# Kernel tuning notes

Hardware: AMD Instinct MI355X
Metric: run time of the kernel (lower is better)

## Reference

```python
import jax, jax.numpy as jnp
import numpy as np


def setup_inputs() -> dict:
    key = jax.random.key(0)
    ks = jax.random.split(key, 7)
    B, C, H, W = 8, 256, 64, 64
    C8 = C // 8
    s = 0.05
    return {
        "x": jax.random.normal(ks[0], (B, C, H, W), dtype=jnp.float32),
        "wq": jax.random.normal(ks[1], (C8, C), dtype=jnp.float32) * s,
        "bq": jax.random.normal(ks[2], (C8,), dtype=jnp.float32) * s,
        "wk": jax.random.normal(ks[3], (C8, C), dtype=jnp.float32) * s,
        "bk": jax.random.normal(ks[4], (C8,), dtype=jnp.float32) * s,
        "wv": jax.random.normal(ks[5], (C, C), dtype=jnp.float32) * s,
        "bv": jax.random.normal(ks[6], (C,), dtype=jnp.float32) * s,
    }


def reference(x, wq, bq, wk, bk, wv, bv):
    B, C, H, W = x.shape
    xf = x.reshape(B, C, H * W)                      # [B, C, N]
    # conv1x1 projections (per-position linear over channels)
    f = jnp.einsum('oc,bcn->bon', wq, xf) + bq[None, :, None]   # [B, C/8, N]
    g = jnp.einsum('oc,bcn->bon', wk, xf) + bk[None, :, None]   # [B, C/8, N]
    h = jnp.einsum('oc,bcn->bon', wv, xf) + bv[None, :, None]   # [B, C,   N]
    # scores[b, n, m] = sum_c f[b,c,n] * g[b,c,m]  == bmm(f^T, g)
    scores = jnp.einsum('bcn,bcm->bnm', f, g)        # [B, N, N]
    # NOTE: original uses softmax over dim=1 (the f/query-position axis)
    beta = jax.nn.softmax(scores, axis=1)            # [B, N, N]
    # o[b, c, m] = sum_n h[b,c,n] * beta[b,n,m]  == bmm(h, beta)
    o = jnp.einsum('bcn,bnm->bcm', h, beta)          # [B, C, N]
    return o.reshape(B, C, H, W)
```

## Files before the change

### kernel.cpp

```cpp
#include <hip/hip_runtime.h>
#include <hip/hip_bf16.h>

typedef __bf16 bf16_t;
typedef __bf16 bf16x8 __attribute__((ext_vector_type(8)));
typedef __bf16 bf16x4 __attribute__((ext_vector_type(4)));
typedef float  f32x4  __attribute__((ext_vector_type(4)));

#define NB  8
#define NC  256
#define NC8 32
#define NN  4096
#define XS  264

#define MFMA16(a, b, c) __builtin_amdgcn_mfma_f32_16x16x32_bf16((a), (b), (c), 0, 0, 0)

__global__ __launch_bounds__(256) void cvt_all(const float* __restrict__ wq,
                                               const float* __restrict__ wk,
                                               const float* __restrict__ wv,
                                               bf16_t* __restrict__ wqb,
                                               bf16_t* __restrict__ wkb,
                                               bf16_t* __restrict__ wvb) {
    int i = blockIdx.x * 256 + threadIdx.x;
    const float* src; bf16_t* dst; int off;
    if (i < 2048)      { src = wq; dst = wqb; off = i; }
    else if (i < 4096) { src = wk; dst = wkb; off = i - 2048; }
    else               { src = wv; dst = wvb; off = i - 4096; }
    float4 v = reinterpret_cast<const float4*>(src)[off];
    bf16x4 o;
    o[0] = (bf16_t)v.x; o[1] = (bf16_t)v.y; o[2] = (bf16_t)v.z; o[3] = (bf16_t)v.w;
    reinterpret_cast<bf16x4*>(dst)[off] = o;
}

__global__ __launch_bounds__(256) void proj_fused(const float* __restrict__ x,
                                                  const bf16_t* __restrict__ wq,
                                                  const float* __restrict__ bq,
                                                  const bf16_t* __restrict__ wk,
                                                  const float* __restrict__ bk,
                                                  const bf16_t* __restrict__ wv,
                                                  const float* __restrict__ bv,
                                                  bf16_t* __restrict__ ft,
                                                  bf16_t* __restrict__ gt,
                                                  bf16_t* __restrict__ h) {
    __shared__ bf16_t tile[64][72];
    __shared__ bf16_t xs[64 * XS];

    const int bx = blockIdx.x;
    const int b  = bx >> 6;
    const int n0 = (bx & 63) * 64;
    const int t  = threadIdx.x;
    const int w    = t >> 6;
    const int lane = t & 63;
    const int q    = lane >> 4;
    const int r    = lane & 15;

    const int cl  = t >> 4;
    const int nl  = (t & 15) * 4;
    const int nb_ = t >> 3;
    const int cl2 = (t & 7) * 8;

    float4 xv[16];
#pragma unroll
    for (int cp = 0; cp < 4; ++cp)
#pragma unroll
        for (int p = 0; p < 4; ++p)
            xv[4 * cp + p] = *reinterpret_cast<const float4*>(
                x + ((size_t)b * NC + 64 * cp + cl + 16 * p) * NN + n0 + nl);

    for (int cp = 0; cp < 4; ++cp) {
#pragma unroll
        for (int p = 0; p < 4; ++p) {
            const int cc = cl + 16 * p;
            float4 v = xv[4 * cp + p];
            bf16x4 bv4;
            bv4[0] = (bf16_t)v.x; bv4[1] = (bf16_t)v.y; bv4[2] = (bf16_t)v.z; bv4[3] = (bf16_t)v.w;
            *reinterpret_cast<bf16x4*>(&tile[cc][nl]) = bv4;
        }
        __syncthreads();
#pragma unroll
        for (int p = 0; p < 2; ++p) {
            const int nn = nb_ + 32 * p;
            bf16x8 v;
            for (int i = 0; i < 8; ++i) v[i] = tile[cl2 + i][nn];
            *reinterpret_cast<bf16x8*>(&xs[nn * XS + 64 * cp + cl2]) = v;
        }
        __syncthreads();
    }

    {
        const bf16_t* xrow = &xs[(16 * w + r) * XS];
        f32x4 accq[2], acck[2];
        for (int ot = 0; ot < 2; ++ot) {
            accq[ot] = (f32x4){0.f, 0.f, 0.f, 0.f};
            acck[ot] = (f32x4){0.f, 0.f, 0.f, 0.f};
        }
        bf16x8 a_c  = *reinterpret_cast<const bf16x8*>(xrow + 8 * q);
        bf16x8 fq_c[2], fk_c[2];
#pragma unroll
        for (int ot = 0; ot < 2; ++ot) {
            fq_c[ot] = *reinterpret_cast<const bf16x8*>(wq + (size_t)(16 * ot + r) * NC + 8 * q);
            fk_c[ot] = *reinterpret_cast<const bf16x8*>(wk + (size_t)(16 * ot + r) * NC + 8 * q);
        }
        for (int k0 = 0; k0 < NC; k0 += 32) {
            const int kn = (k0 + 32 < NC) ? k0 + 32 : 0;
            bf16x8 a_n = *reinterpret_cast<const bf16x8*>(xrow + kn + 8 * q);
            bf16x8 fq_n[2], fk_n[2];
#pragma unroll
            for (int ot = 0; ot < 2; ++ot) {
                fq_n[ot] = *reinterpret_cast<const bf16x8*>(wq + (size_t)(16 * ot + r) * NC + kn + 8 * q);
                fk_n[ot] = *reinterpret_cast<const bf16x8*>(wk + (size_t)(16 * ot + r) * NC + kn + 8 * q);
            }
#pragma unroll
            for (int ot = 0; ot < 2; ++ot) {
                accq[ot] = MFMA16(a_c, fq_c[ot], accq[ot]);
                acck[ot] = MFMA16(a_c, fk_c[ot], acck[ot]);
            }
            a_c = a_n;
#pragma unroll
            for (int ot = 0; ot < 2; ++ot) { fq_c[ot] = fq_n[ot]; fk_c[ot] = fk_n[ot]; }
        }
        for (int ot = 0; ot < 2; ++ot) {
            const int o = 16 * ot + r;
            const float biq = bq[o];
            const float bik = bk[o];
            for (int i = 0; i < 4; ++i) {
                const int n = n0 + 16 * w + 4 * q + i;
                ft[((size_t)b * NN + n) * NC8 + o] = (bf16_t)(accq[ot][i] + biq);
                gt[((size_t)b * NN + n) * NC8 + o] = (bf16_t)(acck[ot][i] + bik);
            }
        }
    }

    f32x4 vacc[4][4];
    for (int ct = 0; ct < 4; ++ct)
        for (int nt = 0; nt < 4; ++nt) vacc[ct][nt] = (f32x4){0.f, 0.f, 0.f, 0.f};

    bf16x8 wv_c[4];
#pragma unroll
    for (int ct = 0; ct < 4; ++ct)
        wv_c[ct] = *reinterpret_cast<const bf16x8*>(
            wv + (size_t)(64 * ct + 16 * w + r) * NC + 8 * q);

    for (int k0 = 0; k0 < NC; k0 += 32) {
        const int kn = (k0 + 32 < NC) ? k0 + 32 : 0;
        bf16x8 wv_n[4];
#pragma unroll
        for (int ct = 0; ct < 4; ++ct)
            wv_n[ct] = *reinterpret_cast<const bf16x8*>(
                wv + (size_t)(64 * ct + 16 * w + r) * NC + kn + 8 * q);
        bf16x8 bfr[4];
#pragma unroll
        for (int nt = 0; nt < 4; ++nt)
            bfr[nt] = *reinterpret_cast<const bf16x8*>(&xs[(16 * nt + r) * XS + k0 + 8 * q]);
#pragma unroll
        for (int ct = 0; ct < 4; ++ct)
#pragma unroll
            for (int nt = 0; nt < 4; ++nt)
                vacc[ct][nt] = MFMA16(wv_c[ct], bfr[nt], vacc[ct][nt]);
#pragma unroll
        for (int ct = 0; ct < 4; ++ct) wv_c[ct] = wv_n[ct];
    }
    for (int ct = 0; ct < 4; ++ct) {
        for (int nt = 0; nt < 4; ++nt) {
            const int n32 = (n0 >> 5) + (nt >> 1);
            const int dn  = 16 * (nt & 1) + r;
            for (int i = 0; i < 4; ++i) {
                const int c = 64 * ct + 16 * w + 4 * q + i;
                h[(((size_t)b * 128 + n32) * NC + c) * 32 + dn] = (bf16_t)(vacc[ct][nt][i] + bv[c]);
            }
        }
    }
}

#define O_STEP(HU, HL, KC, LOFF)                                               \
    {                                                                          \
        _Pragma("unroll")                                                      \
        for (int ct = 0; ct < 2; ++ct)                                         \
            HL[ct] = *reinterpret_cast<const bf16x8*>(                         \
                hrow[ct] + (size_t)(LOFF) * 256);                              \
        bf16x8 pf[4];                                                          \
        _Pragma("unroll")                                                      \
        for (int mt = 0; mt < 4; ++mt) {                                       \
            const int row = 16 * mt + r;                                       \
            pf[mt] = *reinterpret_cast<const bf16x8*>(                         \
                &Pb[(row << 7) + (((4 * (KC) + q) ^ rq) << 3)]);               \
        }                                                                      \
        _Pragma("unroll")                                                      \
        for (int ct = 0; ct < 2; ++ct)                                         \
            _Pragma("unroll")                                                  \
            for (int mt = 0; mt < 4; ++mt)                                     \
                acc[ct][mt] = MFMA16(HU[ct], pf[mt], acc[ct][mt]);             \
    }

__global__ __launch_bounds__(512, 4) void attn(const bf16_t* __restrict__ ft,
                                               const bf16_t* __restrict__ gt,
                                               const bf16_t* __restrict__ h,
                                               float* __restrict__ out) {
    __shared__ bf16_t P[2 * 64 * 128];
    __shared__ float  l_lds[64];

    const int bx = blockIdx.x;
    const int b  = bx & 7;
    const int m0 = (bx >> 3) * 64;
    const int tid  = threadIdx.x;
    const int w    = tid >> 6;
    const int lane = tid & 63;
    const int q    = lane >> 4;
    const int r    = lane & 15;
    const int rq   = r & 7;

    if (tid < 64) l_lds[tid] = 0.f;

    bf16x8 qf[4];
#pragma unroll
    for (int mt = 0; mt < 4; ++mt)
        qf[mt] = *reinterpret_cast<const bf16x8*>(
            gt + ((size_t)b * NN + m0 + 16 * mt + r) * NC8 + 8 * q);

    f32x4 acc[2][4];
#pragma unroll
    for (int ct = 0; ct < 2; ++ct)
#pragma unroll
        for (int mt = 0; mt < 4; ++mt) acc[ct][mt] = (f32x4){0.f, 0.f, 0.f, 0.f};
    float lp[4] = {0.f, 0.f, 0.f, 0.f};

    const bf16_t* fb = ft + (size_t)b * NN * NC8;
    const bf16_t* hb = h + (size_t)b * 128 * NC * 32;
    const f32x4 zero = (f32x4){0.f, 0.f, 0.f, 0.f};

    const bf16_t* hrow[2];
#pragma unroll
    for (int ct = 0; ct < 2; ++ct)
        hrow[ct] = hb + (size_t)(32 * w + 16 * ct + r) * 32 + 8 * q;
    const bf16_t* fptr = fb + (size_t)(16 * w + r) * NC8 + 8 * q;

    f32x4 s[4];
    {
        bf16x8 a0 = *reinterpret_cast<const bf16x8*>(fptr);
#pragma unroll
        for (int mt = 0; mt < 4; ++mt) s[mt] = MFMA16(a0, qf[mt], zero);
    }
    bf16x8 h0[2], h1[2];
#pragma unroll
    for (int ct = 0; ct < 2; ++ct)
        h0[ct] = *reinterpret_cast<const bf16x8*>(hrow[ct]);

    for (int ii = 0; ii < 32; ++ii) {
        bf16_t* Pb = &P[(ii & 1) << 13];
        const int nb = ii * 128;
        const int nld = (ii + 1 < 32 ? ii + 1 : 31) * 128;

        bf16x8 af0 = *reinterpret_cast<const bf16x8*>(fptr + (size_t)nld * NC8);

#pragma unroll
        for (int mt = 0; mt < 4; ++mt) {
            float e0 = __expf(s[mt][0]);
            float e1 = __expf(s[mt][1]);
            float e2 = __expf(s[mt][2]);
            float e3 = __expf(s[mt][3]);
            lp[mt] += (e0 + e1) + (e2 + e3);
            bf16x4 pv;
            pv[0] = (bf16_t)e0; pv[1] = (bf16_t)e1; pv[2] = (bf16_t)e2; pv[3] = (bf16_t)e3;
            const int row  = 16 * mt + r;
            const int nblk = 2 * w + (q >> 1);
            *reinterpret_cast<bf16x4*>(
                &Pb[(row << 7) + ((nblk ^ rq) << 3) + 4 * (q & 1)]) = pv;
        }

        asm volatile("s_waitcnt lgkmcnt(0)" ::: "memory");
        __builtin_amdgcn_sched_barrier(0);
        __builtin_amdgcn_s_barrier();
        __builtin_amdgcn_sched_barrier(0);

        const int nbn = (ii + 1 < 32 ? nb + 128 : nb);
        __builtin_amdgcn_s_setprio(1);
        O_STEP(h0, h1, 0, nb + 32);
        O_STEP(h1, h0, 1, nb + 64);
        O_STEP(h0, h1, 2, nb + 96);
        O_STEP(h1, h0, 3, nbn);

#pragma unroll
        for (int mt = 0; mt < 4; ++mt) s[mt] = MFMA16(af0, qf[mt], zero);
        __builtin_amdgcn_s_setprio(0);
    }

    __syncthreads();
#pragma unroll
    for (int mt = 0; mt < 4; ++mt) {
        float v = lp[mt];
        v += __shfl_xor(v, 16);
        v += __shfl_xor(v, 32);
        if (q == 0) atomicAdd(&l_lds[16 * mt + r], v);
    }
    __syncthreads();

#pragma unroll
    for (int ct = 0; ct < 2; ++ct) {
#pragma unroll
        for (int mt = 0; mt < 4; ++mt) {
            const int m = m0 + 16 * mt + r;
            const float linv = 1.0f / l_lds[16 * mt + r];
#pragma unroll
            for (int i = 0; i < 4; ++i) {
                const int c = 32 * w + 16 * ct + 4 * q + i;
                out[((size_t)b * NC + c) * NN + m] = acc[ct][mt][i] * linv;
            }
        }
    }
}

extern "C" void kernel_launch(void* const* d_in, const int* in_sizes, int n_in,
                              void* d_out, int out_size, void* d_ws, size_t ws_size,
                              hipStream_t stream) {
    const float* x  = (const float*)d_in[0];
    const float* wq = (const float*)d_in[1];
    const float* bq = (const float*)d_in[2];
    const float* wk = (const float*)d_in[3];
    const float* bk = (const float*)d_in[4];
    const float* wv = (const float*)d_in[5];
    const float* bv = (const float*)d_in[6];
    float* out = (float*)d_out;

    bf16_t* ft  = (bf16_t*)d_ws;
    bf16_t* gt  = ft + (size_t)NB * NN * NC8;
    bf16_t* hb  = gt + (size_t)NB * NN * NC8;
    bf16_t* wqb = hb + (size_t)NB * NC * NN;
    bf16_t* wkb = wqb + (size_t)NC8 * NC;
    bf16_t* wvb = wkb + (size_t)NC8 * NC;

    cvt_all<<<80, 256, 0, stream>>>(wq, wk, wv, wqb, wkb, wvb);
    proj_fused<<<NB * (NN / 64), 256, 0, stream>>>(x, wqb, bq, wkb, bk, wvb, bv, ft, gt, hb);
    attn<<<NB * (NN / 64), 512, 0, stream>>>(ft, gt, hb, out);
}
```

Baseline: 191.8 us.

## Split projection into separate transpose kernel and global-memory projection matmul

Moves the x transpose and bf16 conversion out of the fused projection kernel into a dedicated kernel that writes a transposed bf16 copy of x into the output buffer as scratch. The projection kernel then reads its MFMA operands directly from global memory instead of LDS, with register double-buffering of the x fragments. The aim is to cut LDS usage and barrier stalls in the projection kernel so more blocks fit per CU. The cost is an extra kernel launch and a full write and re-read of the transposed x through global memory.

```diff
diff --git a/kernel.cpp b/kernel.cpp
--- a/kernel.cpp
+++ b/kernel.cpp
@@ -31,19 +31,69 @@
     reinterpret_cast<bf16x4*>(dst)[off] = o;
 }
 
-__global__ __launch_bounds__(256) void proj_fused(const float* __restrict__ x,
-                                                  const bf16_t* __restrict__ wq,
-                                                  const float* __restrict__ bq,
-                                                  const bf16_t* __restrict__ wk,
-                                                  const float* __restrict__ bk,
-                                                  const bf16_t* __restrict__ wv,
-                                                  const float* __restrict__ bv,
-                                                  bf16_t* __restrict__ ft,
-                                                  bf16_t* __restrict__ gt,
-                                                  bf16_t* __restrict__ h) {
+__global__ __launch_bounds__(256) void xpose(const float* __restrict__ x,
+                                             bf16_t* __restrict__ xt) {
     __shared__ bf16_t tile[64][72];
     __shared__ bf16_t xs[64 * XS];
 
+    const int bx = blockIdx.x;
+    const int b  = bx >> 6;
+    const int n0 = (bx & 63) * 64;
+    const int t  = threadIdx.x;
+
+    const int cl  = t >> 4;
+    const int nl  = (t & 15) * 4;
+    const int nb_ = t >> 3;
+    const int cl2 = (t & 7) * 8;
+
+    float4 xv[16];
+#pragma unroll
+    for (int cp = 0; cp < 4; ++cp)
+#pragma unroll
+        for (int p = 0; p < 4; ++p)
+            xv[4 * cp + p] = *reinterpret_cast<const float4*>(
+                x + ((size_t)b * NC + 64 * cp + cl + 16 * p) * NN + n0 + nl);
+
+    for (int cp = 0; cp < 4; ++cp) {
+#pragma unroll
+        for (int p = 0; p < 4; ++p) {
+            const int cc = cl + 16 * p;
+            float4 v = xv[4 * cp + p];
+            bf16x4 bv4;
+            bv4[0] = (bf16_t)v.x; bv4[1] = (bf16_t)v.y; bv4[2] = (bf16_t)v.z; bv4[3] = (bf16_t)v.w;
+            *reinterpret_cast<bf16x4*>(&tile[cc][nl]) = bv4;
+        }
+        __syncthreads();
+#pragma unroll
+        for (int p = 0; p < 2; ++p) {
+            const int nn = nb_ + 32 * p;
+            bf16x8 v;
+            for (int i = 0; i < 8; ++i) v[i] = tile[cl2 + i][nn];
+            *reinterpret_cast<bf16x8*>(&xs[nn * XS + 64 * cp + cl2]) = v;
+        }
+        __syncthreads();
+    }
+
+    const int row = t >> 5;
+    const int ch  = t & 31;
+#pragma unroll
+    for (int p = 0; p < 8; ++p) {
+        const int rr = row + 8 * p;
+        bf16x8 v = *reinterpret_cast<const bf16x8*>(&xs[rr * XS + ch * 8]);
+        *reinterpret_cast<bf16x8*>(xt + ((size_t)b * NN + n0 + rr) * NC + ch * 8) = v;
+    }
+}
+
+__global__ __launch_bounds__(256) void projmm(const bf16_t* __restrict__ xt,
+                                              const bf16_t* __restrict__ wq,
+                                              const float* __restrict__ bq,
+                                              const bf16_t* __restrict__ wk,
+                                              const float* __restrict__ bk,
+                                              const bf16_t* __restrict__ wv,
+                                              const float* __restrict__ bv,
+                                              bf16_t* __restrict__ ft,
+                                              bf16_t* __restrict__ gt,
+                                              bf16_t* __restrict__ h) {
     const int bx = blockIdx.x;
     const int b  = bx >> 6;
     const int n0 = (bx & 63) * 64;
@@ -53,41 +103,10 @@
     const int q    = lane >> 4;
     const int r    = lane & 15;
 
-    const int cl  = t >> 4;
-    const int nl  = (t & 15) * 4;
-    const int nb_ = t >> 3;
-    const int cl2 = (t & 7) * 8;
-
-    float4 xv[16];
-#pragma unroll
-    for (int cp = 0; cp < 4; ++cp)
-#pragma unroll
-        for (int p = 0; p < 4; ++p)
-            xv[4 * cp + p] = *reinterpret_cast<const float4*>(
-                x + ((size_t)b * NC + 64 * cp + cl + 16 * p) * NN + n0 + nl);
-
-    for (int cp = 0; cp < 4; ++cp) {
-#pragma unroll
-        for (int p = 0; p < 4; ++p) {
-            const int cc = cl + 16 * p;
-            float4 v = xv[4 * cp + p];
-            bf16x4 bv4;
-            bv4[0] = (bf16_t)v.x; bv4[1] = (bf16_t)v.y; bv4[2] = (bf16_t)v.z; bv4[3] = (bf16_t)v.w;
-            *reinterpret_cast<bf16x4*>(&tile[cc][nl]) = bv4;
-        }
-        __syncthreads();
-#pragma unroll
-        for (int p = 0; p < 2; ++p) {
-            const int nn = nb_ + 32 * p;
-            bf16x8 v;
-            for (int i = 0; i < 8; ++i) v[i] = tile[cl2 + i][nn];
-            *reinterpret_cast<bf16x8*>(&xs[nn * XS + 64 * cp + cl2]) = v;
-        }
-        __syncthreads();
-    }
+    const bf16_t* xb = xt + ((size_t)b * NN + n0) * NC;
 
     {
-        const bf16_t* xrow = &xs[(16 * w + r) * XS];
+        const bf16_t* xrow = xb + (size_t)(16 * w + r) * NC;
         f32x4 accq[2], acck[2];
         for (int ot = 0; ot < 2; ++ot) {
             accq[ot] = (f32x4){0.f, 0.f, 0.f, 0.f};
@@ -134,30 +153,34 @@
     for (int ct = 0; ct < 4; ++ct)
         for (int nt = 0; nt < 4; ++nt) vacc[ct][nt] = (f32x4){0.f, 0.f, 0.f, 0.f};
 
-    bf16x8 wv_c[4];
+    bf16x8 wv_c[4], bfr_c[4];
 #pragma unroll
     for (int ct = 0; ct < 4; ++ct)
         wv_c[ct] = *reinterpret_cast<const bf16x8*>(
             wv + (size_t)(64 * ct + 16 * w + r) * NC + 8 * q);
+#pragma unroll
+    for (int nt = 0; nt < 4; ++nt)
+        bfr_c[nt] = *reinterpret_cast<const bf16x8*>(xb + (size_t)(16 * nt + r) * NC + 8 * q);
 
     for (int k0 = 0; k0 < NC; k0 += 32) {
         const int kn = (k0 + 32 < NC) ? k0 + 32 : 0;
-        bf16x8 wv_n[4];
+        bf16x8 wv_n[4], bfr_n[4];
 #pragma unroll
         for (int ct = 0; ct < 4; ++ct)
             wv_n[ct] = *reinterpret_cast<const bf16x8*>(
                 wv + (size_t)(64 * ct + 16 * w + r) * NC + kn + 8 * q);
-        bf16x8 bfr[4];
 #pragma unroll
         for (int nt = 0; nt < 4; ++nt)
-            bfr[nt] = *reinterpret_cast<const bf16x8*>(&xs[(16 * nt + r) * XS + k0 + 8 * q]);
+            bfr_n[nt] = *reinterpret_cast<const bf16x8*>(xb + (size_t)(16 * nt + r) * NC + kn + 8 * q);
 #pragma unroll
         for (int ct = 0; ct < 4; ++ct)
 #pragma unroll
             for (int nt = 0; nt < 4; ++nt)
-                vacc[ct][nt] = MFMA16(wv_c[ct], bfr[nt], vacc[ct][nt]);
+                vacc[ct][nt] = MFMA16(wv_c[ct], bfr_c[nt], vacc[ct][nt]);
 #pragma unroll
         for (int ct = 0; ct < 4; ++ct) wv_c[ct] = wv_n[ct];
+#pragma unroll
+        for (int nt = 0; nt < 4; ++nt) bfr_c[nt] = bfr_n[nt];
     }
     for (int ct = 0; ct < 4; ++ct) {
         for (int nt = 0; nt < 4; ++nt) {
@@ -327,7 +350,10 @@
     bf16_t* wkb = wqb + (size_t)NC8 * NC;
     bf16_t* wvb = wkb + (size_t)NC8 * NC;
 
+    bf16_t* xT = (bf16_t*)out;
+
     cvt_all<<<80, 256, 0, stream>>>(wq, wk, wv, wqb, wkb, wvb);
-    proj_fused<<<NB * (NN / 64), 256, 0, stream>>>(x, wqb, bq, wkb, bk, wvb, bv, ft, gt, hb);
+    xpose<<<NB * (NN / 64), 256, 0, stream>>>(x, xT);
+    projmm<<<NB * (NN / 64), 256, 0, stream>>>(xT, wqb, bq, wkb, bk, wvb, bv, ft, gt, hb);
     attn<<<NB * (NN / 64), 512, 0, stream>>>(ft, gt, hb, out);
 }
```

Measured after the change: 203.1 us. 5.9% more time.

## Pre-tile bf16 weights and swap MFMA operands for vectorized projection stores

Applied to the files above, without the earlier changes.

The weight conversion kernel now writes bf16 weights in a 16x32 tiled layout, so each lane's 8-element fragment load is contiguous within a tile. The projection kernel swaps the MFMA A/B operands so every lane's accumulators hold four consecutive output channels (q/k) or positions (v), which allows bf16x4 vector stores instead of scalar ones. Weight fragments are prefetched before the x transpose, and the xs LDS fragments are double-buffered. This targets scattered global stores and weight-load latency in the projection stage only, leaving the attention kernel, which is likely the dominant cost, unchanged.

```diff
diff --git a/kernel.cpp b/kernel.cpp
--- a/kernel.cpp
+++ b/kernel.cpp
@@ -13,6 +13,7 @@
 #define XS  264
 
 #define MFMA16(a, b, c) __builtin_amdgcn_mfma_f32_16x16x32_bf16((a), (b), (c), 0, 0, 0)
+
 
 __global__ __launch_bounds__(256) void cvt_all(const float* __restrict__ wq,
                                                const float* __restrict__ wk,
@@ -26,21 +27,25 @@
     else if (i < 4096) { src = wk; dst = wkb; off = i - 2048; }
     else               { src = wv; dst = wvb; off = i - 4096; }
     float4 v = reinterpret_cast<const float4*>(src)[off];
-    bf16x4 o;
-    o[0] = (bf16_t)v.x; o[1] = (bf16_t)v.y; o[2] = (bf16_t)v.z; o[3] = (bf16_t)v.w;
-    reinterpret_cast<bf16x4*>(dst)[off] = o;
+    const int e = off * 4;
+    const int o = e >> 8;
+    const int k = e & 255;
+    const size_t d = (size_t)((o >> 4) * 8 + (k >> 5)) * 512 + (o & 15) * 32 + (k & 31);
+    bf16x4 ov;
+    ov[0] = (bf16_t)v.x; ov[1] = (bf16_t)v.y; ov[2] = (bf16_t)v.z; ov[3] = (bf16_t)v.w;
+    *reinterpret_cast<bf16x4*>(dst + d) = ov;
 }
 
-__global__ __launch_bounds__(256) void proj_fused(const float* __restrict__ x,
-                                                  const bf16_t* __restrict__ wq,
-                                                  const float* __restrict__ bq,
-                                                  const bf16_t* __restrict__ wk,
-                                                  const float* __restrict__ bk,
-                                                  const bf16_t* __restrict__ wv,
-                                                  const float* __restrict__ bv,
-                                                  bf16_t* __restrict__ ft,
-                                                  bf16_t* __restrict__ gt,
-                                                  bf16_t* __restrict__ h) {
+__global__ __launch_bounds__(256) void proj2(const float* __restrict__ x,
+                                             const bf16_t* __restrict__ wq,
+                                             const float* __restrict__ bq,
+                                             const bf16_t* __restrict__ wk,
+                                             const float* __restrict__ bk,
+                                             const bf16_t* __restrict__ wv,
+                                             const float* __restrict__ bv,
+                                             bf16_t* __restrict__ ft,
+                                             bf16_t* __restrict__ gt,
+                                             bf16_t* __restrict__ h) {
     __shared__ bf16_t tile[64][72];
     __shared__ bf16_t xs[64 * XS];
 
@@ -66,6 +71,18 @@
             xv[4 * cp + p] = *reinterpret_cast<const float4*>(
                 x + ((size_t)b * NC + 64 * cp + cl + 16 * p) * NN + n0 + nl);
 
+    const int fo = r * 32 + 8 * q;
+    bf16x8 fq_c[2], fk_c[2], wv_c[4];
+#pragma unroll
+    for (int ot = 0; ot < 2; ++ot) {
+        fq_c[ot] = *reinterpret_cast<const bf16x8*>(wq + ot * 4096 + fo);
+        fk_c[ot] = *reinterpret_cast<const bf16x8*>(wk + ot * 4096 + fo);
+    }
+#pragma unroll
+    for (int ct = 0; ct < 4; ++ct)
+        wv_c[ct] = *reinterpret_cast<const bf16x8*>(
+            wv + (size_t)w * 4096 + (size_t)ct * 16384 + fo);
+
     for (int cp = 0; cp < 4; ++cp) {
 #pragma unroll
         for (int p = 0; p < 4; ++p) {
@@ -93,40 +110,38 @@
             accq[ot] = (f32x4){0.f, 0.f, 0.f, 0.f};
             acck[ot] = (f32x4){0.f, 0.f, 0.f, 0.f};
         }
-        bf16x8 a_c  = *reinterpret_cast<const bf16x8*>(xrow + 8 * q);
-        bf16x8 fq_c[2], fk_c[2];
-#pragma unroll
-        for (int ot = 0; ot < 2; ++ot) {
-            fq_c[ot] = *reinterpret_cast<const bf16x8*>(wq + (size_t)(16 * ot + r) * NC + 8 * q);
-            fk_c[ot] = *reinterpret_cast<const bf16x8*>(wk + (size_t)(16 * ot + r) * NC + 8 * q);
-        }
-        for (int k0 = 0; k0 < NC; k0 += 32) {
-            const int kn = (k0 + 32 < NC) ? k0 + 32 : 0;
-            bf16x8 a_n = *reinterpret_cast<const bf16x8*>(xrow + kn + 8 * q);
+        bf16x8 a_c = *reinterpret_cast<const bf16x8*>(xrow + 8 * q);
+        for (int kp = 0; kp < 8; ++kp) {
+            const int kn = (kp + 1 < 8) ? kp + 1 : 0;
+            bf16x8 a_n = *reinterpret_cast<const bf16x8*>(xrow + kn * 32 + 8 * q);
             bf16x8 fq_n[2], fk_n[2];
 #pragma unroll
             for (int ot = 0; ot < 2; ++ot) {
-                fq_n[ot] = *reinterpret_cast<const bf16x8*>(wq + (size_t)(16 * ot + r) * NC + kn + 8 * q);
-                fk_n[ot] = *reinterpret_cast<const bf16x8*>(wk + (size_t)(16 * ot + r) * NC + kn + 8 * q);
+                fq_n[ot] = *reinterpret_cast<const bf16x8*>(wq + ot * 4096 + kn * 512 + fo);
+                fk_n[ot] = *reinterpret_cast<const bf16x8*>(wk + ot * 4096 + kn * 512 + fo);
             }
 #pragma unroll
             for (int ot = 0; ot < 2; ++ot) {
-                accq[ot] = MFMA16(a_c, fq_c[ot], accq[ot]);
-                acck[ot] = MFMA16(a_c, fk_c[ot], acck[ot]);
+                accq[ot] = MFMA16(fq_c[ot], a_c, accq[ot]);
+                acck[ot] = MFMA16(fk_c[ot], a_c, acck[ot]);
             }
             a_c = a_n;
 #pragma unroll
             for (int ot = 0; ot < 2; ++ot) { fq_c[ot] = fq_n[ot]; fk_c[ot] = fk_n[ot]; }
         }
+        const int n = n0 + 16 * w + r;
+#pragma unroll
         for (int ot = 0; ot < 2; ++ot) {
-            const int o = 16 * ot + r;
-            const float biq = bq[o];
-            const float bik = bk[o];
-            for (int i = 0; i < 4; ++i) {
-                const int n = n0 + 16 * w + 4 * q + i;
-                ft[((size_t)b * NN + n) * NC8 + o] = (bf16_t)(accq[ot][i] + biq);
-                gt[((size_t)b * NN + n) * NC8 + o] = (bf16_t)(acck[ot][i] + bik);
-            }
+            const int o4 = 16 * ot + 4 * q;
+            float4 b4q = *reinterpret_cast<const float4*>(bq + o4);
+            float4 b4k = *reinterpret_cast<const float4*>(bk + o4);
+            bf16x4 pq, pk;
+            pq[0] = (bf16_t)(accq[ot][0] + b4q.x); pq[1] = (bf16_t)(accq[ot][1] + b4q.y);
+            pq[2] = (bf16_t)(accq[ot][2] + b4q.z); pq[3] = (bf16_t)(accq[ot][3] + b4q.w);
+            pk[0] = (bf16_t)(acck[ot][0] + b4k.x); pk[1] = (bf16_t)(acck[ot][1] + b4k.y);
+            pk[2] = (bf16_t)(acck[ot][2] + b4k.z); pk[3] = (bf16_t)(acck[ot][3] + b4k.w);
+            *reinterpret_cast<bf16x4*>(ft + ((size_t)b * NN + n) * NC8 + o4) = pq;
+            *reinterpret_cast<bf16x4*>(gt + ((size_t)b * NN + n) * NC8 + o4) = pk;
         }
     }
 
@@ -134,39 +149,47 @@
     for (int ct = 0; ct < 4; ++ct)
         for (int nt = 0; nt < 4; ++nt) vacc[ct][nt] = (f32x4){0.f, 0.f, 0.f, 0.f};
 
-    bf16x8 wv_c[4];
-#pragma unroll
-    for (int ct = 0; ct < 4; ++ct)
-        wv_c[ct] = *reinterpret_cast<const bf16x8*>(
-            wv + (size_t)(64 * ct + 16 * w + r) * NC + 8 * q);
-
-    for (int k0 = 0; k0 < NC; k0 += 32) {
-        const int kn = (k0 + 32 < NC) ? k0 + 32 : 0;
-        bf16x8 wv_n[4];
+    bf16x8 bfr_c[4];
+#pragma unroll
+    for (int nt = 0; nt < 4; ++nt)
+        bfr_c[nt] = *reinterpret_cast<const bf16x8*>(&xs[(16 * nt + r) * XS + 8 * q]);
+
+    for (int kp = 0; kp < 8; ++kp) {
+        const int kn = (kp + 1 < 8) ? kp + 1 : 0;
+        bf16x8 wv_n[4], bfr_n[4];
 #pragma unroll
         for (int ct = 0; ct < 4; ++ct)
             wv_n[ct] = *reinterpret_cast<const bf16x8*>(
-                wv + (size_t)(64 * ct + 16 * w + r) * NC + kn + 8 * q);
-        bf16x8 bfr[4];
+                wv + (size_t)w * 4096 + (size_t)ct * 16384 + kn * 512 + fo);
 #pragma unroll
         for (int nt = 0; nt < 4; ++nt)
-            bfr[nt] = *reinterpret_cast<const bf16x8*>(&xs[(16 * nt + r) * XS + k0 + 8 * q]);
+            bfr_n[nt] = *reinterpret_cast<const bf16x8*>(&xs[(16 * nt + r) * XS + kn * 32 + 8 * q]);
 #pragma unroll
         for (int ct = 0; ct < 4; ++ct)
 #pragma unroll
             for (int nt = 0; nt < 4; ++nt)
-                vacc[ct][nt] = MFMA16(wv_c[ct], bfr[nt], vacc[ct][nt]);
+                vacc[ct][nt] = MFMA16(bfr_c[nt], wv_c[ct], vacc[ct][nt]);
 #pragma unroll
         for (int ct = 0; ct < 4; ++ct) wv_c[ct] = wv_n[ct];
-    }
+#pragma unroll
+        for (int nt = 0; nt < 4; ++nt) bfr_c[nt] = bfr_n[nt];
+    }
+
+#pragma unroll
     for (int ct = 0; ct < 4; ++ct) {
+        const int c = 64 * ct + 16 * w + r;
+        const float bvc = bv[c];
+#pragma unroll
         for (int nt = 0; nt < 4; ++nt) {
             const int n32 = (n0 >> 5) + (nt >> 1);
-            const int dn  = 16 * (nt & 1) + r;
-            for (int i = 0; i < 4; ++i) {
-                const int c = 64 * ct + 16 * w + 4 * q + i;
-                h[(((size_t)b * 128 + n32) * NC + c) * 32 + dn] = (bf16_t)(vacc[ct][nt][i] + bv[c]);
-            }
+            const int dn0 = 16 * (nt & 1) + 4 * q;
+            bf16x4 pv;
+            pv[0] = (bf16_t)(vacc[ct][nt][0] + bvc);
+            pv[1] = (bf16_t)(vacc[ct][nt][1] + bvc);
+            pv[2] = (bf16_t)(vacc[ct][nt][2] + bvc);
+            pv[3] = (bf16_t)(vacc[ct][nt][3] + bvc);
+            *reinterpret_cast<bf16x4*>(
+                h + (((size_t)b * 128 + n32) * NC + c) * 32 + dn0) = pv;
         }
     }
 }
@@ -328,6 +351,6 @@
     bf16_t* wvb = wkb + (size_t)NC8 * NC;
 
     cvt_all<<<80, 256, 0, stream>>>(wq, wk, wv, wqb, wkb, wvb);
-    proj_fused<<<NB * (NN / 64), 256, 0, stream>>>(x, wqb, bq, wkb, bk, wvb, bv, ft, gt, hb);
+    proj2<<<NB * (NN / 64), 256, 0, stream>>>(x, wqb, bq, wkb, bk, wvb, bv, ft, gt, hb);
     attn<<<NB * (NN / 64), 512, 0, stream>>>(ft, gt, hb, out);
 }
```

After: 188.1 us. About the same (-1.9%).
